# Kernel tuning notes

Hardware: AMD Instinct MI355X
Metric: run time of the kernel (lower is better)

Reference implementation:

```python
import jax, jax.numpy as jnp
import numpy as np

N_NODES = 100000
N_EDGES = 1600000
IN_FEATS, HIDDEN_FEATS, OUT_FEATS = 32, 64, 16


def setup_inputs() -> dict:
    key = jax.random.key(0)
    ks = jax.random.split(key, 8)
    return {
        "features": jax.random.normal(ks[0], (N_NODES, IN_FEATS), dtype=jnp.float32),
        "src": jax.random.randint(ks[1], (N_EDGES,), 0, N_NODES, dtype=jnp.int64),
        "dst": jax.random.randint(ks[2], (N_EDGES,), 0, N_NODES, dtype=jnp.int64),
        "W1_self": jax.random.normal(ks[3], (IN_FEATS, HIDDEN_FEATS), dtype=jnp.float32) * 0.1,
        "W1_neigh": jax.random.normal(ks[4], (IN_FEATS, HIDDEN_FEATS), dtype=jnp.float32) * 0.1,
        "b1": jnp.zeros((HIDDEN_FEATS,), dtype=jnp.float32),
        "W2_self": jax.random.normal(ks[5], (HIDDEN_FEATS, OUT_FEATS), dtype=jnp.float32) * 0.1,
        "W2_neigh": jax.random.normal(ks[6], (HIDDEN_FEATS, OUT_FEATS), dtype=jnp.float32) * 0.1,
        "b2": jnp.zeros((OUT_FEATS,), dtype=jnp.float32),
    }


def _sage_conv_mean(h, src, dst, n_nodes, W_self, W_neigh, b):
    # DGL SAGEConv(mean): gather src features to edges, mean-reduce at dst,
    # then fc_self(h) + fc_neigh(mean_neigh) + bias.
    ones = jnp.ones(src.shape, dtype=h.dtype)
    deg = jax.ops.segment_sum(ones, dst, num_segments=n_nodes)  # in-degree [N]
    agg = jax.ops.segment_sum(h[src], dst, num_segments=n_nodes)  # [N, d]
    mean_neigh = agg / jnp.maximum(deg, 1.0)[:, None]
    return h @ W_self + mean_neigh @ W_neigh + b


def reference(features, src, dst, W1_self, W1_neigh, b1, W2_self, W2_neigh, b2):
    n = features.shape[0]
    h = _sage_conv_mean(features, src, dst, n, W1_self, W1_neigh, b1)
    h = jax.nn.relu(h)
    # dropout is identity at inference (Keras call default training=False)
    out = _sage_conv_mean(h, src, dst, n, W2_self, W2_neigh, b2)
    return out
```

## Files before the change

### kernel.cpp

```cpp
#include <hip/hip_runtime.h>

#define N_NODES 100000
#define N_EDGES 1600000
#define IN_F 32
#define HID_F 64
#define OUT_F 16
#define BSIZE 512
#define NBKT 256
#define CAP 10240
#define CHUNK 4096
#define NBUCK ((N_NODES + BSIZE - 1) / BSIZE)
#define NCHUNK ((N_EDGES + CHUNK - 1) / CHUNK)
#define CAPN 48
#define APITCH 68

using f2v = __attribute__((ext_vector_type(2))) float;

#define ADDQ(s, Q) do { f2v p_; \
  p_ = __builtin_amdgcn_cvt_pk_f32_fp8((int)(Q).x, false); s[0] += p_[0]; s[1] += p_[1]; \
  p_ = __builtin_amdgcn_cvt_pk_f32_fp8((int)(Q).x, true);  s[2] += p_[0]; s[3] += p_[1]; \
  p_ = __builtin_amdgcn_cvt_pk_f32_fp8((int)(Q).y, false); s[4] += p_[0]; s[5] += p_[1]; \
  p_ = __builtin_amdgcn_cvt_pk_f32_fp8((int)(Q).y, true);  s[6] += p_[0]; s[7] += p_[1]; \
  p_ = __builtin_amdgcn_cvt_pk_f32_fp8((int)(Q).z, false); s[8] += p_[0]; s[9] += p_[1]; \
  p_ = __builtin_amdgcn_cvt_pk_f32_fp8((int)(Q).z, true);  s[10] += p_[0]; s[11] += p_[1]; \
  p_ = __builtin_amdgcn_cvt_pk_f32_fp8((int)(Q).w, false); s[12] += p_[0]; s[13] += p_[1]; \
  p_ = __builtin_amdgcn_cvt_pk_f32_fp8((int)(Q).w, true);  s[14] += p_[0]; s[15] += p_[1]; \
} while (0)

__global__ __launch_bounds__(NBKT) void cursor_init_kernel(int* __restrict__ cursor) {
  cursor[threadIdx.x] = threadIdx.x * CAP;
}

__global__ __launch_bounds__(512) void bucket_kernel(
    const int* __restrict__ src, const int* __restrict__ dst,
    const float4* __restrict__ featin, uint4* __restrict__ featfp8,
    int* __restrict__ cursor, unsigned* __restrict__ sorted) {
  __shared__ unsigned stage[CHUNK];
  __shared__ unsigned char sbkt[CHUNK];
  __shared__ int lcnt[NBKT], lscan[NBKT], goff[NBKT];
  __shared__ int wsum[4];
  int t = threadIdx.x;

  {
    int gtid = blockIdx.x * 512 + t;
    if (gtid < N_NODES * IN_F / 16) {
      float4 a = featin[4 * gtid], bb = featin[4 * gtid + 1];
      float4 c4 = featin[4 * gtid + 2], d = featin[4 * gtid + 3];
      uint4 r;
      int w;
      w = __builtin_amdgcn_cvt_pk_fp8_f32(a.x, a.y, 0, false);
      w = __builtin_amdgcn_cvt_pk_fp8_f32(a.z, a.w, w, true);
      r.x = (unsigned)w;
      w = __builtin_amdgcn_cvt_pk_fp8_f32(bb.x, bb.y, 0, false);
      w = __builtin_amdgcn_cvt_pk_fp8_f32(bb.z, bb.w, w, true);
      r.y = (unsigned)w;
      w = __builtin_amdgcn_cvt_pk_fp8_f32(c4.x, c4.y, 0, false);
      w = __builtin_amdgcn_cvt_pk_fp8_f32(c4.z, c4.w, w, true);
      r.z = (unsigned)w;
      w = __builtin_amdgcn_cvt_pk_fp8_f32(d.x, d.y, 0, false);
      w = __builtin_amdgcn_cvt_pk_fp8_f32(d.z, d.w, w, true);
      r.w = (unsigned)w;
      featfp8[gtid] = r;
    }
  }

  if (t < NBKT) lcnt[t] = 0;
  __syncthreads();

  int base = blockIdx.x * CHUNK;
  unsigned mypk[CHUNK / 512];
  int myb[CHUNK / 512], myrank[CHUNK / 512];
#pragma unroll
  for (int i = 0; i < CHUNK / 512; ++i) {
    int e = base + t + 512 * i;
    if (e < N_EDGES) {
      unsigned s = (unsigned)src[e], d = (unsigned)dst[e];
      myb[i] = (int)(d >> 9);
      mypk[i] = (s << 9) | (d & 511u);
      myrank[i] = atomicAdd(&lcnt[myb[i]], 1);
    } else {
      myb[i] = -1;
    }
  }
  __syncthreads();

  int x = 0;
  if (t < NBKT) {
    x = lcnt[t];
#pragma unroll
    for (int off = 1; off < 64; off <<= 1) {
      int y = __shfl_up(x, off);
      if ((t & 63) >= off) x += y;
    }
    if ((t & 63) == 63) wsum[t >> 6] = x;
  }
  __syncthreads();
  if (t < NBKT) {
    int w = t >> 6, add = 0;
    if (w > 0) add += wsum[0];
    if (w > 1) add += wsum[1];
    if (w > 2) add += wsum[2];
    int incl = x + add;
    lscan[t] = incl;
    int gb = lcnt[t] ? atomicAdd(&cursor[t], lcnt[t]) : 0;
    goff[t] = gb - incl + lcnt[t];
  }
  __syncthreads();

#pragma unroll
  for (int i = 0; i < CHUNK / 512; ++i) {
    if (myb[i] >= 0) {
      int slot = (lscan[myb[i]] - lcnt[myb[i]]) + myrank[i];
      stage[slot] = mypk[i];
      sbkt[slot] = (unsigned char)myb[i];
    }
  }
  __syncthreads();
  int nvalid = min(CHUNK, N_EDGES - base);
  for (int i = t; i < nvalid; i += 512) {
    int b = (int)sbkt[i];
    sorted[goff[b] + i] = stage[i];
  }
}

__global__ __launch_bounds__(1024) void csr_kernel(
    const unsigned* __restrict__ sorted, const int* __restrict__ cursor,
    int* __restrict__ cnt, int* __restrict__ col) {
  __shared__ int dcnt[BSIZE];
  int t = threadIdx.x;
  int b = blockIdx.x;
  if (t < BSIZE) dcnt[t] = 0;
  __syncthreads();

  int cbase = b * CAP;
  int ne = cursor[b] - cbase;
  const uint4* S4 = (const uint4*)(sorted + cbase);
  int nv4 = ne >> 2;
  for (int i = t; i < nv4; i += 1024) {
    uint4 pp = S4[i];
    int d0 = (int)(pp.x & (BSIZE - 1)), r0 = atomicAdd(&dcnt[d0], 1);
    int d1 = (int)(pp.y & (BSIZE - 1)), r1 = atomicAdd(&dcnt[d1], 1);
    int d2 = (int)(pp.z & (BSIZE - 1)), r2 = atomicAdd(&dcnt[d2], 1);
    int d3 = (int)(pp.w & (BSIZE - 1)), r3 = atomicAdd(&dcnt[d3], 1);
    if (r0 < CAPN) col[(b * BSIZE + d0) * CAPN + r0] = (int)(pp.x >> 9);
    if (r1 < CAPN) col[(b * BSIZE + d1) * CAPN + r1] = (int)(pp.y >> 9);
    if (r2 < CAPN) col[(b * BSIZE + d2) * CAPN + r2] = (int)(pp.z >> 9);
    if (r3 < CAPN) col[(b * BSIZE + d3) * CAPN + r3] = (int)(pp.w >> 9);
  }
  {
    int rem = ne & 3;
    if (t < rem) {
      unsigned p = sorted[cbase + (nv4 << 2) + t];
      int d = (int)(p & (BSIZE - 1));
      int r = atomicAdd(&dcnt[d], 1);
      if (r < CAPN) col[(b * BSIZE + d) * CAPN + r] = (int)(p >> 9);
    }
  }
  __syncthreads();
  if (t < BSIZE) {
    int v = b * BSIZE + t;
    if (v < N_NODES) cnt[v] = dcnt[t];
  }
}

__global__ __launch_bounds__(256) void l1g_kernel(
    const float* __restrict__ feat, const uint4* __restrict__ featfp8,
    const int* __restrict__ cnt, const int* __restrict__ col,
    const float* __restrict__ W1s, const float* __restrict__ W1n,
    const float* __restrict__ b1,
    const float* __restrict__ W2n, const float* __restrict__ W2s,
    unsigned* __restrict__ t2f8, float* __restrict__ s2) {
  __shared__ float sA[64 * APITCH];
  __shared__ float sW[64 * 32];

  int t = threadIdx.x;
  int tile = blockIdx.x * 64;
  int nvalid = min(64, N_NODES - tile);

  const float4* Fg = (const float4*)(feat + (size_t)tile * IN_F);
  int lim = nvalid * 8;
  int fi0 = t, fi1 = t + 256;
  float4 fa0, fa1;
  if (fi0 < lim) fa0 = Fg[fi0];
  if (fi1 < lim) fa1 = Fg[fi1];
  int wrow = t >> 3, wq = t & 7;
  const float4* srcw0 = (wrow < 32) ? (const float4*)W1s : (const float4*)W1n;
  int wrow1 = (t + 256) >> 3, wq1 = (t + 256) & 7;
  const float4* srcw1 = (wrow1 < 32) ? (const float4*)W1s : (const float4*)W1n;
  float4 wa0 = srcw0[(wrow & 31) * 16 + wq];
  float4 wa1 = srcw1[(wrow1 & 31) * 16 + wq1];

  {
    int nl = t >> 2, c = (t >> 1) & 1, hp = t & 1;
    int v = tile + nl;
    if (nl < nvalid) {
      int deg = cnt[v];
      int start = v * CAPN;
      int dclamp = min(deg, CAPN);
      int end = start + dclamp;
      float s[16];
#pragma unroll
      for (int j = 0; j < 16; ++j) s[j] = 0.0f;
      int nf = dclamp & ~7;
      for (int g = 0; g < nf; g += 8) {
        int4 cc = *(const int4*)&col[start + g + 4 * hp];
        uint4 q0 = featfp8[cc.x * 2 + c];
        uint4 q1 = featfp8[cc.y * 2 + c];
        uint4 q2 = featfp8[cc.z * 2 + c];
        uint4 q3 = featfp8[cc.w * 2 + c];
        ADDQ(s, q0);
        ADDQ(s, q1);
        ADDQ(s, q2);
        ADDQ(s, q3);
      }
      for (int e = start + nf + hp; e < end; e += 2) {
        uint4 q = featfp8[col[e] * 2 + c];
        ADDQ(s, q);
      }
#pragma unroll
      for (int j = 0; j < 16; ++j) s[j] += __shfl_xor(s[j], 1);
      float inv = 1.0f / fmaxf((float)deg, 1.0f);
      int j0 = 8 * hp;
#pragma unroll
      for (int j = 0; j < 8; ++j)
        sA[(32 + 16 * c + j0 + j) * APITCH + nl] = s[j0 + j] * inv;
    }
  }

  if (fi0 < lim) {
    int n = fi0 >> 3, c8 = fi0 & 7;
    sA[(4 * c8 + 0) * APITCH + n] = fa0.x;
    sA[(4 * c8 + 1) * APITCH + n] = fa0.y;
    sA[(4 * c8 + 2) * APITCH + n] = fa0.z;
    sA[(4 * c8 + 3) * APITCH + n] = fa0.w;
  }
  if (fi1 < lim) {
    int n = fi1 >> 3, c8 = fi1 & 7;
    sA[(4 * c8 + 0) * APITCH + n] = fa1.x;
    sA[(4 * c8 + 1) * APITCH + n] = fa1.y;
    sA[(4 * c8 + 2) * APITCH + n] = fa1.z;
    sA[(4 * c8 + 3) * APITCH + n] = fa1.w;
  }
  {
    float4* Ws = (float4*)sW;
    Ws[t] = wa0;
    Ws[t + 256] = wa1;
  }
  float4 wb0 = srcw0[(wrow & 31) * 16 + 8 + wq];
  float4 wb1 = srcw1[(wrow1 & 31) * 16 + 8 + wq1];

  int tx = t & 15, ty = t >> 4;
  int n0 = 4 * ty, cA = 2 * tx;
  float2 bbA = ((const float2*)b1)[tx];
  float2 bbB = ((const float2*)b1)[16 + tx];
  __syncthreads();

  float aA[4][2], aB[4][2];
#pragma unroll
  for (int i = 0; i < 4; ++i) {
    aA[i][0] = bbA.x; aA[i][1] = bbA.y;
    aB[i][0] = bbB.x; aB[i][1] = bbB.y;
  }
#pragma unroll 4
  for (int k = 0; k < 64; ++k) {
    float4 a = *(const float4*)&sA[k * APITCH + n0];
    float2 w = *(const float2*)&sW[k * 32 + cA];
    aA[0][0] += a.x * w.x; aA[0][1] += a.x * w.y;
    aA[1][0] += a.y * w.x; aA[1][1] += a.y * w.y;
    aA[2][0] += a.z * w.x; aA[2][1] += a.z * w.y;
    aA[3][0] += a.w * w.x; aA[3][1] += a.w * w.y;
  }
  __syncthreads();
  {
    float4* Ws = (float4*)sW;
    Ws[t] = wb0;
    Ws[t + 256] = wb1;
  }
  __syncthreads();

#pragma unroll 4
  for (int k = 0; k < 64; ++k) {
    float4 a = *(const float4*)&sA[k * APITCH + n0];
    float2 w = *(const float2*)&sW[k * 32 + cA];
    aB[0][0] += a.x * w.x; aB[0][1] += a.x * w.y;
    aB[1][0] += a.y * w.x; aB[1][1] += a.y * w.y;
    aB[2][0] += a.z * w.x; aB[2][1] += a.z * w.y;
    aB[3][0] += a.w * w.x; aB[3][1] += a.w * w.y;
  }
  __syncthreads();

#pragma unroll
  for (int j = 0; j < 2; ++j) {
    float4 v;
    v.x = fmaxf(aA[0][j], 0.0f);
    v.y = fmaxf(aA[1][j], 0.0f);
    v.z = fmaxf(aA[2][j], 0.0f);
    v.w = fmaxf(aA[3][j], 0.0f);
    *(float4*)&sA[(cA + j) * APITCH + n0] = v;
    float4 u;
    u.x = fmaxf(aB[0][j], 0.0f);
    u.y = fmaxf(aB[1][j], 0.0f);
    u.z = fmaxf(aB[2][j], 0.0f);
    u.w = fmaxf(aB[3][j], 0.0f);
    *(float4*)&sA[(32 + cA + j) * APITCH + n0] = u;
  }
  {
    float4* Ws = (float4*)sW;
#pragma unroll
    for (int it = 0; it < 2; ++it) {
      int idx = t + 256 * it;
      int row = idx >> 3, ch = idx & 7;
      const float4* srcw = (ch < 4) ? (const float4*)W2n : (const float4*)W2s;
      Ws[row * 8 + ch] = srcw[row * 4 + (ch & 3)];
    }
  }
  __syncthreads();

  int c2 = cA;
  float a0 = 0.f, a1 = 0.f, b0 = 0.f, b1_ = 0.f, d0 = 0.f, d1 = 0.f, e0 = 0.f, e1 = 0.f;
#pragma unroll 4
  for (int k = 0; k < 64; ++k) {
    float4 a = *(const float4*)&sA[k * APITCH + n0];
    float2 w = *(const float2*)&sW[k * 32 + c2];
    a0 += a.x * w.x; a1 += a.x * w.y;
    b0 += a.y * w.x; b1_ += a.y * w.y;
    d0 += a.z * w.x; d1 += a.z * w.y;
    e0 += a.w * w.x; e1 += a.w * w.y;
  }
  {
    float rs[4][2] = {{a0, a1}, {b0, b1_}, {d0, d1}, {e0, e1}};
    int cc = c2 & 15;
#pragma unroll
    for (int i = 0; i < 4; ++i) {
      int v = tile + n0 + i;
      if (v < N_NODES) {
        if (c2 < 16) {
          int w = __builtin_amdgcn_cvt_pk_fp8_f32(rs[i][0], rs[i][1], 0, false);
          *(unsigned short*)((char*)t2f8 + (size_t)v * 16 + cc) = (unsigned short)w;
        } else {
          *(float2*)&s2[v * OUT_F + cc] = make_float2(rs[i][0], rs[i][1]);
        }
      }
    }
  }
}

__global__ __launch_bounds__(256) void gather2_final_kernel(
    const int* __restrict__ cnt, const int* __restrict__ col,
    const uint4* __restrict__ t2f8, const float* __restrict__ s2,
    const float* __restrict__ b2, float* __restrict__ out) {
  int g = blockIdx.x * 256 + threadIdx.x;
  int v = g >> 2, hp = g & 3;
  if (v >= N_NODES) return;
  int deg = cnt[v];
  int start = v * CAPN;
  int dclamp = min(deg, CAPN);
  int end = start + dclamp;
  float s[16];
#pragma unroll
  for (int j = 0; j < 16; ++j) s[j] = 0.0f;
  int nf = dclamp & ~15;
  for (int gg = 0; gg < nf; gg += 16) {
    int4 cc = *(const int4*)&col[start + gg + 4 * hp];
    uint4 q0 = t2f8[cc.x];
    uint4 q1 = t2f8[cc.y];
    uint4 q2 = t2f8[cc.z];
    uint4 q3 = t2f8[cc.w];
    ADDQ(s, q0);
    ADDQ(s, q1);
    ADDQ(s, q2);
    ADDQ(s, q3);
  }
  int e0 = start + nf;
  if (dclamp - nf >= 8) {
    int2 cc = *(const int2*)&col[e0 + 2 * hp];
    uint4 q0 = t2f8[cc.x];
    uint4 q1 = t2f8[cc.y];
    ADDQ(s, q0);
    ADDQ(s, q1);
    e0 += 8;
  }
  for (int e = e0 + hp; e < end; e += 4) {
    uint4 q = t2f8[col[e]];
    ADDQ(s, q);
  }
#pragma unroll
  for (int j = 0; j < 16; ++j) s[j] += __shfl_xor(s[j], 1);
#pragma unroll
  for (int j = 0; j < 16; ++j) s[j] += __shfl_xor(s[j], 2);
  float inv = 1.0f / fmaxf((float)deg, 1.0f);
  float q0 = (hp == 0) ? s[0]  : (hp == 1) ? s[4]  : (hp == 2) ? s[8]  : s[12];
  float q1 = (hp == 0) ? s[1]  : (hp == 1) ? s[5]  : (hp == 2) ? s[9]  : s[13];
  float q2 = (hp == 0) ? s[2]  : (hp == 1) ? s[6]  : (hp == 2) ? s[10] : s[14];
  float q3 = (hp == 0) ? s[3]  : (hp == 1) ? s[7]  : (hp == 2) ? s[11] : s[15];
  float4 sv = ((const float4*)s2)[v * 4 + hp];
  float4 bv = ((const float4*)b2)[hp];
  float4 r;
  r.x = sv.x + bv.x + q0 * inv;
  r.y = sv.y + bv.y + q1 * inv;
  r.z = sv.z + bv.z + q2 * inv;
  r.w = sv.w + bv.w + q3 * inv;
  ((float4*)out)[v * 4 + hp] = r;
}

extern "C" void kernel_launch(void* const* d_in, const int* in_sizes, int n_in,
                              void* d_out, int out_size, void* d_ws, size_t ws_size,
                              hipStream_t stream) {
  const float* feat = (const float*)d_in[0];
  const int* src    = (const int*)d_in[1];
  const int* dst    = (const int*)d_in[2];
  const float* W1s  = (const float*)d_in[3];
  const float* W1n  = (const float*)d_in[4];
  const float* b1   = (const float*)d_in[5];
  const float* W2s  = (const float*)d_in[6];
  const float* W2n  = (const float*)d_in[7];
  const float* b2   = (const float*)d_in[8];
  float* out = (float*)d_out;

  const size_t N = N_NODES;
  const size_t SLAB = (size_t)NBUCK * CAP;
  int* cnt = (int*)d_ws;
  int* col = cnt + N + 16;
  unsigned* sorted = (unsigned*)(col + N * CAPN + 16);
  float* s2 = (float*)sorted;
  unsigned* featfp8 = (unsigned*)(sorted + SLAB + 16);
  unsigned* t2f8 = featfp8 + 8 * N;
  int* cursor = (int*)(t2f8 + 4 * N);

  cursor_init_kernel<<<1, NBKT, 0, stream>>>(cursor);
  bucket_kernel<<<NCHUNK, 512, 0, stream>>>(
      src, dst, (const float4*)feat, (uint4*)featfp8, cursor, sorted);
  csr_kernel<<<NBUCK, 1024, 0, stream>>>(sorted, cursor, cnt, col);
  l1g_kernel<<<(N_NODES + 63) / 64, 256, 0, stream>>>(
      feat, (const uint4*)featfp8, cnt, col, W1s, W1n, b1, W2n, W2s, t2f8, s2);
  gather2_final_kernel<<<(4 * N_NODES + 255) / 256, 256, 0, stream>>>(
      cnt, col, (const uint4*)t2f8, s2, b2, out);
}
```

Baseline: 163.6 us.

## Replace padded CSR gathers with per-bucket LDS atomic scatter aggregation

Removes the CSR build (per-node padded col lists) and instead aggregates neighbour features directly from the dst-bucketed edge list into shared-memory float accumulators using LDS atomicAdd, for both layers. Layer-1 means are written as bf16 and read back by the dense kernel, replacing its gather loop; layer 2 fuses aggregation with the final bias and self term add. This cuts the col write and read traffic and the CAPN truncation, at the cost of many shared-memory float atomics per edge (32 or 16 per edge) and large LDS use per block, which limits occupancy.

```diff
diff --git a/kernel.cpp b/kernel.cpp
--- a/kernel.cpp
+++ b/kernel.cpp
@@ -11,20 +11,26 @@
 #define CHUNK 4096
 #define NBUCK ((N_NODES + BSIZE - 1) / BSIZE)
 #define NCHUNK ((N_EDGES + CHUNK - 1) / CHUNK)
-#define CAPN 48
 #define APITCH 68
+#define AP1 33
+#define AP2 17
 
 using f2v = __attribute__((ext_vector_type(2))) float;
 
-#define ADDQ(s, Q) do { f2v p_; \
-  p_ = __builtin_amdgcn_cvt_pk_f32_fp8((int)(Q).x, false); s[0] += p_[0]; s[1] += p_[1]; \
-  p_ = __builtin_amdgcn_cvt_pk_f32_fp8((int)(Q).x, true);  s[2] += p_[0]; s[3] += p_[1]; \
-  p_ = __builtin_amdgcn_cvt_pk_f32_fp8((int)(Q).y, false); s[4] += p_[0]; s[5] += p_[1]; \
-  p_ = __builtin_amdgcn_cvt_pk_f32_fp8((int)(Q).y, true);  s[6] += p_[0]; s[7] += p_[1]; \
-  p_ = __builtin_amdgcn_cvt_pk_f32_fp8((int)(Q).z, false); s[8] += p_[0]; s[9] += p_[1]; \
-  p_ = __builtin_amdgcn_cvt_pk_f32_fp8((int)(Q).z, true);  s[10] += p_[0]; s[11] += p_[1]; \
-  p_ = __builtin_amdgcn_cvt_pk_f32_fp8((int)(Q).w, false); s[12] += p_[0]; s[13] += p_[1]; \
-  p_ = __builtin_amdgcn_cvt_pk_f32_fp8((int)(Q).w, true);  s[14] += p_[0]; s[15] += p_[1]; \
+__device__ __forceinline__ unsigned f2bf(float f) {
+  unsigned u = __float_as_uint(f);
+  return (u + 0x7FFFu + ((u >> 16) & 1u)) >> 16;
+}
+
+#define ADDQL(ap, Q, off) do { f2v p_; \
+  p_ = __builtin_amdgcn_cvt_pk_f32_fp8((int)(Q).x, false); atomicAdd((ap)+(off)+0,  p_[0]); atomicAdd((ap)+(off)+1,  p_[1]); \
+  p_ = __builtin_amdgcn_cvt_pk_f32_fp8((int)(Q).x, true);  atomicAdd((ap)+(off)+2,  p_[0]); atomicAdd((ap)+(off)+3,  p_[1]); \
+  p_ = __builtin_amdgcn_cvt_pk_f32_fp8((int)(Q).y, false); atomicAdd((ap)+(off)+4,  p_[0]); atomicAdd((ap)+(off)+5,  p_[1]); \
+  p_ = __builtin_amdgcn_cvt_pk_f32_fp8((int)(Q).y, true);  atomicAdd((ap)+(off)+6,  p_[0]); atomicAdd((ap)+(off)+7,  p_[1]); \
+  p_ = __builtin_amdgcn_cvt_pk_f32_fp8((int)(Q).z, false); atomicAdd((ap)+(off)+8,  p_[0]); atomicAdd((ap)+(off)+9,  p_[1]); \
+  p_ = __builtin_amdgcn_cvt_pk_f32_fp8((int)(Q).z, true);  atomicAdd((ap)+(off)+10, p_[0]); atomicAdd((ap)+(off)+11, p_[1]); \
+  p_ = __builtin_amdgcn_cvt_pk_f32_fp8((int)(Q).w, false); atomicAdd((ap)+(off)+12, p_[0]); atomicAdd((ap)+(off)+13, p_[1]); \
+  p_ = __builtin_amdgcn_cvt_pk_f32_fp8((int)(Q).w, true);  atomicAdd((ap)+(off)+14, p_[0]); atomicAdd((ap)+(off)+15, p_[1]); \
 } while (0)
 
 __global__ __launch_bounds__(NBKT) void cursor_init_kernel(int* __restrict__ cursor) {
@@ -123,49 +129,52 @@
   }
 }
 
-__global__ __launch_bounds__(1024) void csr_kernel(
+__global__ __launch_bounds__(1024) void agg1_kernel(
     const unsigned* __restrict__ sorted, const int* __restrict__ cursor,
-    int* __restrict__ cnt, int* __restrict__ col) {
+    const uint4* __restrict__ featfp8, uint4* __restrict__ meanb) {
+  __shared__ float acc[BSIZE * AP1];
   __shared__ int dcnt[BSIZE];
   int t = threadIdx.x;
   int b = blockIdx.x;
+  for (int i = t; i < BSIZE * AP1; i += 1024) acc[i] = 0.0f;
   if (t < BSIZE) dcnt[t] = 0;
   __syncthreads();
 
   int cbase = b * CAP;
   int ne = cursor[b] - cbase;
-  const uint4* S4 = (const uint4*)(sorted + cbase);
-  int nv4 = ne >> 2;
-  for (int i = t; i < nv4; i += 1024) {
-    uint4 pp = S4[i];
-    int d0 = (int)(pp.x & (BSIZE - 1)), r0 = atomicAdd(&dcnt[d0], 1);
-    int d1 = (int)(pp.y & (BSIZE - 1)), r1 = atomicAdd(&dcnt[d1], 1);
-    int d2 = (int)(pp.z & (BSIZE - 1)), r2 = atomicAdd(&dcnt[d2], 1);
-    int d3 = (int)(pp.w & (BSIZE - 1)), r3 = atomicAdd(&dcnt[d3], 1);
-    if (r0 < CAPN) col[(b * BSIZE + d0) * CAPN + r0] = (int)(pp.x >> 9);
-    if (r1 < CAPN) col[(b * BSIZE + d1) * CAPN + r1] = (int)(pp.y >> 9);
-    if (r2 < CAPN) col[(b * BSIZE + d2) * CAPN + r2] = (int)(pp.z >> 9);
-    if (r3 < CAPN) col[(b * BSIZE + d3) * CAPN + r3] = (int)(pp.w >> 9);
-  }
-  {
-    int rem = ne & 3;
-    if (t < rem) {
-      unsigned p = sorted[cbase + (nv4 << 2) + t];
-      int d = (int)(p & (BSIZE - 1));
-      int r = atomicAdd(&dcnt[d], 1);
-      if (r < CAPN) col[(b * BSIZE + d) * CAPN + r] = (int)(p >> 9);
-    }
-  }
-  __syncthreads();
-  if (t < BSIZE) {
-    int v = b * BSIZE + t;
-    if (v < N_NODES) cnt[v] = dcnt[t];
+  for (int i = t; i < ne; i += 1024) {
+    unsigned p = sorted[cbase + i];
+    int d = (int)(p & (BSIZE - 1));
+    int sv = (int)(p >> 9);
+    uint4 q0 = featfp8[sv * 2];
+    uint4 q1 = featfp8[sv * 2 + 1];
+    atomicAdd(&dcnt[d], 1);
+    float* ap = &acc[d * AP1];
+    ADDQL(ap, q0, 0);
+    ADDQL(ap, q1, 16);
+  }
+  __syncthreads();
+
+  int n = t >> 1, h = t & 1;
+  int v = b * BSIZE + n;
+  if (v < N_NODES) {
+    float inv = 1.0f / fmaxf((float)dcnt[n], 1.0f);
+    const float* ap = &acc[n * AP1 + 16 * h];
+    unsigned w0 = f2bf(ap[0] * inv)  | (f2bf(ap[1] * inv) << 16);
+    unsigned w1 = f2bf(ap[2] * inv)  | (f2bf(ap[3] * inv) << 16);
+    unsigned w2 = f2bf(ap[4] * inv)  | (f2bf(ap[5] * inv) << 16);
+    unsigned w3 = f2bf(ap[6] * inv)  | (f2bf(ap[7] * inv) << 16);
+    unsigned w4 = f2bf(ap[8] * inv)  | (f2bf(ap[9] * inv) << 16);
+    unsigned w5 = f2bf(ap[10] * inv) | (f2bf(ap[11] * inv) << 16);
+    unsigned w6 = f2bf(ap[12] * inv) | (f2bf(ap[13] * inv) << 16);
+    unsigned w7 = f2bf(ap[14] * inv) | (f2bf(ap[15] * inv) << 16);
+    meanb[v * 4 + 2 * h]     = make_uint4(w0, w1, w2, w3);
+    meanb[v * 4 + 2 * h + 1] = make_uint4(w4, w5, w6, w7);
   }
 }
 
 __global__ __launch_bounds__(256) void l1g_kernel(
-    const float* __restrict__ feat, const uint4* __restrict__ featfp8,
-    const int* __restrict__ cnt, const int* __restrict__ col,
+    const float* __restrict__ feat, const uint4* __restrict__ meanb,
     const float* __restrict__ W1s, const float* __restrict__ W1n,
     const float* __restrict__ b1,
     const float* __restrict__ W2n, const float* __restrict__ W2s,
@@ -191,39 +200,19 @@
   float4 wa1 = srcw1[(wrow1 & 31) * 16 + wq1];
 
   {
-    int nl = t >> 2, c = (t >> 1) & 1, hp = t & 1;
+    int nl = t >> 2, q = t & 3;
     int v = tile + nl;
     if (nl < nvalid) {
-      int deg = cnt[v];
-      int start = v * CAPN;
-      int dclamp = min(deg, CAPN);
-      int end = start + dclamp;
-      float s[16];
-#pragma unroll
-      for (int j = 0; j < 16; ++j) s[j] = 0.0f;
-      int nf = dclamp & ~7;
-      for (int g = 0; g < nf; g += 8) {
-        int4 cc = *(const int4*)&col[start + g + 4 * hp];
-        uint4 q0 = featfp8[cc.x * 2 + c];
-        uint4 q1 = featfp8[cc.y * 2 + c];
-        uint4 q2 = featfp8[cc.z * 2 + c];
-        uint4 q3 = featfp8[cc.w * 2 + c];
-        ADDQ(s, q0);
-        ADDQ(s, q1);
-        ADDQ(s, q2);
-        ADDQ(s, q3);
-      }
-      for (int e = start + nf + hp; e < end; e += 2) {
-        uint4 q = featfp8[col[e] * 2 + c];
-        ADDQ(s, q);
-      }
-#pragma unroll
-      for (int j = 0; j < 16; ++j) s[j] += __shfl_xor(s[j], 1);
-      float inv = 1.0f / fmaxf((float)deg, 1.0f);
-      int j0 = 8 * hp;
-#pragma unroll
-      for (int j = 0; j < 8; ++j)
-        sA[(32 + 16 * c + j0 + j) * APITCH + nl] = s[j0 + j] * inv;
+      uint4 mb = meanb[v * 4 + q];
+      int j0 = 8 * q;
+      sA[(32 + j0 + 0) * APITCH + nl] = __uint_as_float(mb.x << 16);
+      sA[(32 + j0 + 1) * APITCH + nl] = __uint_as_float(mb.x & 0xFFFF0000u);
+      sA[(32 + j0 + 2) * APITCH + nl] = __uint_as_float(mb.y << 16);
+      sA[(32 + j0 + 3) * APITCH + nl] = __uint_as_float(mb.y & 0xFFFF0000u);
+      sA[(32 + j0 + 4) * APITCH + nl] = __uint_as_float(mb.z << 16);
+      sA[(32 + j0 + 5) * APITCH + nl] = __uint_as_float(mb.z & 0xFFFF0000u);
+      sA[(32 + j0 + 6) * APITCH + nl] = __uint_as_float(mb.w << 16);
+      sA[(32 + j0 + 7) * APITCH + nl] = __uint_as_float(mb.w & 0xFFFF0000u);
     }
   }
 
@@ -345,62 +334,52 @@
   }
 }
 
-__global__ __launch_bounds__(256) void gather2_final_kernel(
-    const int* __restrict__ cnt, const int* __restrict__ col,
+__global__ __launch_bounds__(1024) void agg2_kernel(
+    const unsigned* __restrict__ sorted, const int* __restrict__ cursor,
     const uint4* __restrict__ t2f8, const float* __restrict__ s2,
     const float* __restrict__ b2, float* __restrict__ out) {
-  int g = blockIdx.x * 256 + threadIdx.x;
-  int v = g >> 2, hp = g & 3;
-  if (v >= N_NODES) return;
-  int deg = cnt[v];
-  int start = v * CAPN;
-  int dclamp = min(deg, CAPN);
-  int end = start + dclamp;
-  float s[16];
-#pragma unroll
-  for (int j = 0; j < 16; ++j) s[j] = 0.0f;
-  int nf = dclamp & ~15;
-  for (int gg = 0; gg < nf; gg += 16) {
-    int4 cc = *(const int4*)&col[start + gg + 4 * hp];
-    uint4 q0 = t2f8[cc.x];
-    uint4 q1 = t2f8[cc.y];
-    uint4 q2 = t2f8[cc.z];
-    uint4 q3 = t2f8[cc.w];
-    ADDQ(s, q0);
-    ADDQ(s, q1);
-    ADDQ(s, q2);
-    ADDQ(s, q3);
-  }
-  int e0 = start + nf;
-  if (dclamp - nf >= 8) {
-    int2 cc = *(const int2*)&col[e0 + 2 * hp];
-    uint4 q0 = t2f8[cc.x];
-    uint4 q1 = t2f8[cc.y];
-    ADDQ(s, q0);
-    ADDQ(s, q1);
-    e0 += 8;
-  }
-  for (int e = e0 + hp; e < end; e += 4) {
-    uint4 q = t2f8[col[e]];
-    ADDQ(s, q);
-  }
-#pragma unroll
-  for (int j = 0; j < 16; ++j) s[j] += __shfl_xor(s[j], 1);
-#pragma unroll
-  for (int j = 0; j < 16; ++j) s[j] += __shfl_xor(s[j], 2);
-  float inv = 1.0f / fmaxf((float)deg, 1.0f);
-  float q0 = (hp == 0) ? s[0]  : (hp == 1) ? s[4]  : (hp == 2) ? s[8]  : s[12];
-  float q1 = (hp == 0) ? s[1]  : (hp == 1) ? s[5]  : (hp == 2) ? s[9]  : s[13];
-  float q2 = (hp == 0) ? s[2]  : (hp == 1) ? s[6]  : (hp == 2) ? s[10] : s[14];
-  float q3 = (hp == 0) ? s[3]  : (hp == 1) ? s[7]  : (hp == 2) ? s[11] : s[15];
-  float4 sv = ((const float4*)s2)[v * 4 + hp];
-  float4 bv = ((const float4*)b2)[hp];
-  float4 r;
-  r.x = sv.x + bv.x + q0 * inv;
-  r.y = sv.y + bv.y + q1 * inv;
-  r.z = sv.z + bv.z + q2 * inv;
-  r.w = sv.w + bv.w + q3 * inv;
-  ((float4*)out)[v * 4 + hp] = r;
+  __shared__ float acc[BSIZE * AP2];
+  __shared__ int dcnt[BSIZE];
+  int t = threadIdx.x;
+  int b = blockIdx.x;
+  for (int i = t; i < BSIZE * AP2; i += 1024) acc[i] = 0.0f;
+  if (t < BSIZE) dcnt[t] = 0;
+  __syncthreads();
+
+  int cbase = b * CAP;
+  int ne = cursor[b] - cbase;
+  for (int i = t; i < ne; i += 1024) {
+    unsigned p = sorted[cbase + i];
+    int d = (int)(p & (BSIZE - 1));
+    int sv = (int)(p >> 9);
+    uint4 q = t2f8[sv];
+    atomicAdd(&dcnt[d], 1);
+    float* ap = &acc[d * AP2];
+    ADDQL(ap, q, 0);
+  }
+  __syncthreads();
+
+  int n = t >> 1, h = t & 1;
+  int v = b * BSIZE + n;
+  if (v < N_NODES) {
+    float inv = 1.0f / fmaxf((float)dcnt[n], 1.0f);
+    const float* ap = &acc[n * AP2 + 8 * h];
+    const float4* S = (const float4*)s2;
+    const float4* B = (const float4*)b2;
+    float4* O = (float4*)out;
+#pragma unroll
+    for (int i = 0; i < 2; ++i) {
+      int ii = 2 * h + i;
+      float4 sv = S[v * 4 + ii];
+      float4 bv = B[ii];
+      float4 r;
+      r.x = sv.x + bv.x + ap[4 * i + 0] * inv;
+      r.y = sv.y + bv.y + ap[4 * i + 1] * inv;
+      r.z = sv.z + bv.z + ap[4 * i + 2] * inv;
+      r.w = sv.w + bv.w + ap[4 * i + 3] * inv;
+      O[v * 4 + ii] = r;
+    }
+  }
 }
 
 extern "C" void kernel_launch(void* const* d_in, const int* in_sizes, int n_in,
@@ -419,20 +398,20 @@
 
   const size_t N = N_NODES;
   const size_t SLAB = (size_t)NBUCK * CAP;
-  int* cnt = (int*)d_ws;
-  int* col = cnt + N + 16;
-  unsigned* sorted = (unsigned*)(col + N * CAPN + 16);
-  float* s2 = (float*)sorted;
-  unsigned* featfp8 = (unsigned*)(sorted + SLAB + 16);
-  unsigned* t2f8 = featfp8 + 8 * N;
-  int* cursor = (int*)(t2f8 + 4 * N);
+  unsigned* sorted = (unsigned*)d_ws;
+  unsigned* featfp8 = sorted + SLAB + 16;
+  unsigned* meanb = featfp8 + 8 * N + 16;
+  unsigned* t2f8 = meanb + 16 * N + 16;
+  float* s2 = (float*)(t2f8 + 4 * N + 16);
+  int* cursor = (int*)(s2 + 16 * N + 16);
 
   cursor_init_kernel<<<1, NBKT, 0, stream>>>(cursor);
   bucket_kernel<<<NCHUNK, 512, 0, stream>>>(
       src, dst, (const float4*)feat, (uint4*)featfp8, cursor, sorted);
-  csr_kernel<<<NBUCK, 1024, 0, stream>>>(sorted, cursor, cnt, col);
+  agg1_kernel<<<NBUCK, 1024, 0, stream>>>(
+      sorted, cursor, (const uint4*)featfp8, (uint4*)meanb);
   l1g_kernel<<<(N_NODES + 63) / 64, 256, 0, stream>>>(
-      feat, (const uint4*)featfp8, cnt, col, W1s, W1n, b1, W2n, W2s, t2f8, s2);
-  gather2_final_kernel<<<(4 * N_NODES + 255) / 256, 256, 0, stream>>>(
-      cnt, col, (const uint4*)t2f8, s2, b2, out);
-}
+      feat, (const uint4*)meanb, W1s, W1n, b1, W2n, W2s, t2f8, s2);
+  agg2_kernel<<<NBUCK, 1024, 0, stream>>>(
+      sorted, cursor, (const uint4*)t2f8, s2, b2, out);
+}
```

Result: slower. 643.7 us (+293.5%).

## Replace global atomic bucket cursors with per-chunk histograms read by CSR kernel

Applied to the files above, without the earlier changes.

The bucket kernel no longer claims global slots with atomics into fixed-capacity bucket slabs. Each chunk now writes its locally sorted edges in place plus an inclusive per-bucket histogram. The CSR kernel walks every chunk's segment for its bucket using two threads per chunk. This drops the cursor init launch and the global atomics, and it removes any overflow risk from the fixed slab capacity. In exchange, each CSR block reads 391 small, scattered segments (about 16 edges each), and only 782 of its 1024 threads do any work.

```diff
diff --git a/kernel.cpp b/kernel.cpp
--- a/kernel.cpp
+++ b/kernel.cpp
@@ -7,7 +7,6 @@
 #define OUT_F 16
 #define BSIZE 512
 #define NBKT 256
-#define CAP 10240
 #define CHUNK 4096
 #define NBUCK ((N_NODES + BSIZE - 1) / BSIZE)
 #define NCHUNK ((N_EDGES + CHUNK - 1) / CHUNK)
@@ -27,17 +26,12 @@
   p_ = __builtin_amdgcn_cvt_pk_f32_fp8((int)(Q).w, true);  s[14] += p_[0]; s[15] += p_[1]; \
 } while (0)
 
-__global__ __launch_bounds__(NBKT) void cursor_init_kernel(int* __restrict__ cursor) {
-  cursor[threadIdx.x] = threadIdx.x * CAP;
-}
-
 __global__ __launch_bounds__(512) void bucket_kernel(
     const int* __restrict__ src, const int* __restrict__ dst,
     const float4* __restrict__ featin, uint4* __restrict__ featfp8,
-    int* __restrict__ cursor, unsigned* __restrict__ sorted) {
+    unsigned* __restrict__ sorted, int* __restrict__ hist) {
   __shared__ unsigned stage[CHUNK];
-  __shared__ unsigned char sbkt[CHUNK];
-  __shared__ int lcnt[NBKT], lscan[NBKT], goff[NBKT];
+  __shared__ int lcnt[NBKT], lscan[NBKT];
   __shared__ int wsum[4];
   int t = threadIdx.x;
 
@@ -102,8 +96,7 @@
     if (w > 2) add += wsum[2];
     int incl = x + add;
     lscan[t] = incl;
-    int gb = lcnt[t] ? atomicAdd(&cursor[t], lcnt[t]) : 0;
-    goff[t] = gb - incl + lcnt[t];
+    hist[blockIdx.x * NBKT + t] = incl;
   }
   __syncthreads();
 
@@ -112,19 +105,16 @@
     if (myb[i] >= 0) {
       int slot = (lscan[myb[i]] - lcnt[myb[i]]) + myrank[i];
       stage[slot] = mypk[i];
-      sbkt[slot] = (unsigned char)myb[i];
     }
   }
   __syncthreads();
   int nvalid = min(CHUNK, N_EDGES - base);
-  for (int i = t; i < nvalid; i += 512) {
-    int b = (int)sbkt[i];
-    sorted[goff[b] + i] = stage[i];
-  }
+  for (int i = t; i < nvalid; i += 512)
+    sorted[base + i] = stage[i];
 }
 
 __global__ __launch_bounds__(1024) void csr_kernel(
-    const unsigned* __restrict__ sorted, const int* __restrict__ cursor,
+    const unsigned* __restrict__ sorted, const int* __restrict__ hist,
     int* __restrict__ cnt, int* __restrict__ col) {
   __shared__ int dcnt[BSIZE];
   int t = threadIdx.x;
@@ -132,25 +122,13 @@
   if (t < BSIZE) dcnt[t] = 0;
   __syncthreads();
 
-  int cbase = b * CAP;
-  int ne = cursor[b] - cbase;
-  const uint4* S4 = (const uint4*)(sorted + cbase);
-  int nv4 = ne >> 2;
-  for (int i = t; i < nv4; i += 1024) {
-    uint4 pp = S4[i];
-    int d0 = (int)(pp.x & (BSIZE - 1)), r0 = atomicAdd(&dcnt[d0], 1);
-    int d1 = (int)(pp.y & (BSIZE - 1)), r1 = atomicAdd(&dcnt[d1], 1);
-    int d2 = (int)(pp.z & (BSIZE - 1)), r2 = atomicAdd(&dcnt[d2], 1);
-    int d3 = (int)(pp.w & (BSIZE - 1)), r3 = atomicAdd(&dcnt[d3], 1);
-    if (r0 < CAPN) col[(b * BSIZE + d0) * CAPN + r0] = (int)(pp.x >> 9);
-    if (r1 < CAPN) col[(b * BSIZE + d1) * CAPN + r1] = (int)(pp.y >> 9);
-    if (r2 < CAPN) col[(b * BSIZE + d2) * CAPN + r2] = (int)(pp.z >> 9);
-    if (r3 < CAPN) col[(b * BSIZE + d3) * CAPN + r3] = (int)(pp.w >> 9);
-  }
-  {
-    int rem = ne & 3;
-    if (t < rem) {
-      unsigned p = sorted[cbase + (nv4 << 2) + t];
+  if (t < 2 * NCHUNK) {
+    int c = t >> 1, h = t & 1;
+    int s0 = b ? hist[c * NBKT + b - 1] : 0;
+    int e0 = hist[c * NBKT + b];
+    int cb = c * CHUNK;
+    for (int i = s0 + h; i < e0; i += 2) {
+      unsigned p = sorted[cb + i];
       int d = (int)(p & (BSIZE - 1));
       int r = atomicAdd(&dcnt[d], 1);
       if (r < CAPN) col[(b * BSIZE + d) * CAPN + r] = (int)(p >> 9);
@@ -418,19 +396,18 @@
   float* out = (float*)d_out;
 
   const size_t N = N_NODES;
-  const size_t SLAB = (size_t)NBUCK * CAP;
+  const size_t SSZ = (size_t)NCHUNK * CHUNK;
   int* cnt = (int*)d_ws;
   int* col = cnt + N + 16;
   unsigned* sorted = (unsigned*)(col + N * CAPN + 16);
   float* s2 = (float*)sorted;
-  unsigned* featfp8 = (unsigned*)(sorted + SLAB + 16);
+  int* hist = (int*)(sorted + SSZ + 16);
+  unsigned* featfp8 = (unsigned*)(hist + NCHUNK * NBKT + 16);
   unsigned* t2f8 = featfp8 + 8 * N;
-  int* cursor = (int*)(t2f8 + 4 * N);
-
-  cursor_init_kernel<<<1, NBKT, 0, stream>>>(cursor);
+
   bucket_kernel<<<NCHUNK, 512, 0, stream>>>(
-      src, dst, (const float4*)feat, (uint4*)featfp8, cursor, sorted);
-  csr_kernel<<<NBUCK, 1024, 0, stream>>>(sorted, cursor, cnt, col);
+      src, dst, (const float4*)feat, (uint4*)featfp8, sorted, hist);
+  csr_kernel<<<NBUCK, 1024, 0, stream>>>(sorted, hist, cnt, col);
   l1g_kernel<<<(N_NODES + 63) / 64, 256, 0, stream>>>(
       feat, (const uint4*)featfp8, cnt, col, W1s, W1n, b1, W2n, W2s, t2f8, s2);
   gather2_final_kernel<<<(4 * N_NODES + 255) / 256, 256, 0, stream>>>(
```

Result: no change. 164.6 us (+0.6%).
